# Kernel optimization log

Hardware: AMD Instinct MI355X
Metric: run time of the kernel (lower is better)

## Reference

```python
import jax, jax.numpy as jnp
import numpy as np
from jax import lax

K = 7          # neighborhood kernel size
NUM_HEADS = 4
EPS = 1e-5


def layernorm(x, w, b):
    mu = x.mean(-1, keepdims=True)
    var = ((x - mu) ** 2).mean(-1, keepdims=True)
    return (x - mu) * lax.rsqrt(var + EPS) * w + b


def window_idx(n, k):
    # NATTEN border behavior: window is shifted (not shrunk) at edges.
    start = jnp.clip(jnp.arange(n) - k // 2, 0, n - k)
    return start[:, None] + jnp.arange(k)  # [n, k]


def neighborhood_attention(x, qkv_w, qkv_b, rpb, proj_w, proj_b):
    B, H, W, C = x.shape
    nh, k = NUM_HEADS, K
    hd = C // nh
    scale = hd ** -0.5
    qkv = (x @ qkv_w + qkv_b).reshape(B, H, W, 3, nh, hd)
    q = jnp.transpose(qkv[:, :, :, 0], (0, 3, 1, 2, 4)) * scale  # [B,nh,H,W,hd]
    kk = jnp.transpose(qkv[:, :, :, 1], (0, 3, 1, 2, 4))
    vv = jnp.transpose(qkv[:, :, :, 2], (0, 3, 1, 2, 4))

    ri = window_idx(H, k)  # [H,k]
    ci = window_idx(W, k)  # [W,k]

    def gather(t):  # [B,nh,H,W,hd] -> [B,nh,H,W,k,k,hd]
        t = t[:, :, ri]           # [B,nh,H,k,W,hd]
        t = t[:, :, :, :, ci]     # [B,nh,H,k,W,k,hd]
        return jnp.transpose(t, (0, 1, 2, 4, 3, 5, 6))

    k_nb = gather(kk)
    v_nb = gather(vv).reshape(B, nh, H, W, k * k, hd)

    attn = jnp.einsum('bnhwd,bnhwijd->bnhwij', q, k_nb)  # [B,nh,H,W,k,k]

    # relative positional bias, rpb: [nh, 2k-1, 2k-1]
    br = ri - jnp.arange(H)[:, None] + (k - 1)  # [H,k] in [0, 2k-2]
    bc = ci - jnp.arange(W)[:, None] + (k - 1)  # [W,k]
    bias = rpb[:, br]                 # [nh,H,k,2k-1]
    bias = bias[:, :, :, bc]          # [nh,H,k,W,k]
    bias = jnp.transpose(bias, (0, 1, 3, 2, 4))  # [nh,H,W,k,k]

    attn = jax.nn.softmax((attn + bias[None]).reshape(B, nh, H, W, k * k), axis=-1)
    out = jnp.einsum('bnhwl,bnhwld->bnhwd', attn, v_nb)
    out = jnp.transpose(out, (0, 2, 3, 1, 4)).reshape(B, H, W, C)
    return out @ proj_w + proj_b


def mlp(x, w1, b1, w2, b2):
    return jax.nn.gelu(x @ w1 + b1, approximate=False) @ w2 + b2


def nat_block_forward(x, norm1_w, norm1_b, qkv_w, qkv_b, rpb, proj_w, proj_b,
                      norm2_w, norm2_b, fc1_w, fc1_b, fc2_w, fc2_b,
                      conv_w, dnorm_w, dnorm_b):
    depth = norm1_w.shape[0]
    for i in range(depth):
        h = layernorm(x, norm1_w[i], norm1_b[i])
        h = neighborhood_attention(h, qkv_w[i], qkv_b[i], rpb[i], proj_w[i], proj_b[i])
        x = x + h
        x = x + mlp(layernorm(x, norm2_w[i], norm2_b[i]),
                    fc1_w[i], fc1_b[i], fc2_w[i], fc2_b[i])
    # ConvDownsampler: 3x3 stride-2 conv (no bias) + LayerNorm, channels-last
    y = lax.conv_general_dilated(x, conv_w, (2, 2), ((1, 1), (1, 1)),
                                 dimension_numbers=('NHWC', 'HWIO', 'NHWC'))
    y = layernorm(y, dnorm_w, dnorm_b)
    return (y, x)


def setup_inputs() -> dict:
    key = jax.random.key(0)
    ks = jax.random.split(key, 12)
    B, H, W, C = 2, 56, 56, 128
    depth, nh, k = 2, NUM_HEADS, K
    hidden = 4 * C
    init = lambda kk, shape: jax.random.normal(kk, shape, jnp.float32) * 0.02
    return {
        'x': jax.random.normal(ks[0], (B, H, W, C), jnp.float32),
        'norm1_w': jnp.ones((depth, C), jnp.float32),
        'norm1_b': jnp.zeros((depth, C), jnp.float32),
        'qkv_w': init(ks[1], (depth, C, 3 * C)),
        'qkv_b': jnp.zeros((depth, 3 * C), jnp.float32),
        'rpb': init(ks[2], (depth, nh, 2 * k - 1, 2 * k - 1)),
        'proj_w': init(ks[3], (depth, C, C)),
        'proj_b': jnp.zeros((depth, C), jnp.float32),
        'norm2_w': jnp.ones((depth, C), jnp.float32),
        'norm2_b': jnp.zeros((depth, C), jnp.float32),
        'fc1_w': init(ks[4], (depth, C, hidden)),
        'fc1_b': jnp.zeros((depth, hidden), jnp.float32),
        'fc2_w': init(ks[5], (depth, hidden, C)),
        'fc2_b': jnp.zeros((depth, C), jnp.float32),
        'conv_w': init(ks[6], (3, 3, C, 2 * C)),
        'dnorm_w': jnp.ones((2 * C,), jnp.float32),
        'dnorm_b': jnp.zeros((2 * C,), jnp.float32),
    }


def reference(x, norm1_w, norm1_b, qkv_w, qkv_b, rpb, proj_w, proj_b,
              norm2_w, norm2_b, fc1_w, fc1_b, fc2_w, fc2_b,
              conv_w, dnorm_w, dnorm_b):
    return nat_block_forward(x, norm1_w, norm1_b, qkv_w, qkv_b, rpb, proj_w,
                             proj_b, norm2_w, norm2_b, fc1_w, fc1_b, fc2_w,
                             fc2_b, conv_w, dnorm_w, dnorm_b)
```

## Files before the change

kernel.cpp:

```cpp
#include <hip/hip_runtime.h>
#include <stdint.h>


typedef __attribute__((ext_vector_type(8))) short bf16x8;
typedef __attribute__((ext_vector_type(4))) float f32x4;

__device__ __forceinline__ float bf2f(uint16_t u) {
  union { uint32_t u; float f; } t;
  t.u = (uint32_t)u << 16;
  return t.f;
}
__device__ __forceinline__ uint16_t f2bf(float f) {
  union { float f; uint32_t u; } t;
  t.f = f;
  return (uint16_t)((t.u + 0x7FFFu + ((t.u >> 16) & 1u)) >> 16);
}

struct PrepArgs {
  const float* src[9];
  uint16_t* dst[9];
  int K[9], N[9];
  int cum[10];
};

__global__ __launch_bounds__(256) void prep_weights(PrepArgs a) {
  __shared__ float t[32][33];
  int bt = blockIdx.x;
  int j = 0;
#pragma unroll
  for (int u = 0; u < 9; ++u)
    if (bt >= a.cum[u + 1]) j = u + 1;
  int lt = bt - a.cum[j];
  const float* w = a.src[j];
  uint16_t* wt = a.dst[j];
  int K = a.K[j], N = a.N[j];
  int tn = N >> 5;
  int n0 = (lt % tn) * 32, k0 = (lt / tn) * 32;
  int tx = threadIdx.x & 31, ty = threadIdx.x >> 5;
#pragma unroll
  for (int r2 = 0; r2 < 32; r2 += 8)
    t[ty + r2][tx] = w[(size_t)(k0 + ty + r2) * N + n0 + tx];
  __syncthreads();
#pragma unroll
  for (int r2 = 0; r2 < 32; r2 += 8)
    wt[(size_t)(n0 + ty + r2) * K + k0 + tx] = f2bf(t[tx][ty + r2]);
}

__global__ __launch_bounds__(256) void ln256_kernel(const float* __restrict__ p0,
                                                    const float* __restrict__ p1,
                                                    const float* __restrict__ p2,
                                                    float* __restrict__ out,
                                                    const float* __restrict__ w,
                                                    const float* __restrict__ b) {
  int wave = threadIdx.x >> 6, lane = threadIdx.x & 63;
  int pix = blockIdx.x * 4 + wave;
  size_t base = (size_t)pix * 256;
  float v0 = p0[base + lane] + p1[base + lane] + p2[base + lane];
  float v1 = p0[base + lane + 64] + p1[base + lane + 64] + p2[base + lane + 64];
  float v2 = p0[base + lane + 128] + p1[base + lane + 128] + p2[base + lane + 128];
  float v3 = p0[base + lane + 192] + p1[base + lane + 192] + p2[base + lane + 192];
  float s = v0 + v1 + v2 + v3;
  float s2 = v0 * v0 + v1 * v1 + v2 * v2 + v3 * v3;
#pragma unroll
  for (int off = 32; off; off >>= 1) {
    s += __shfl_xor(s, off, 64);
    s2 += __shfl_xor(s2, off, 64);
  }
  float mu = s * (1.f / 256.f);
  float var = s2 * (1.f / 256.f) - mu * mu;
  float r = rsqrtf(var + 1e-5f);
  float* q = out + base;
  q[lane] = (v0 - mu) * r * w[lane] + b[lane];
  q[lane + 64] = (v1 - mu) * r * w[lane + 64] + b[lane + 64];
  q[lane + 128] = (v2 - mu) * r * w[lane + 128] + b[lane + 128];
  q[lane + 192] = (v3 - mu) * r * w[lane + 192] + b[lane + 192];
}

template <int KD, int ND, int ACT, int RES, int OUTB, int LNF>
__global__ __launch_bounds__(256) void mfma_gemm32(
    const uint16_t* __restrict__ A, const float* __restrict__ Af,
    const float* __restrict__ lnw, const float* __restrict__ lnb,
    const uint16_t* __restrict__ Wt, const float* __restrict__ bias,
    const float* __restrict__ res, float* __restrict__ outf,
    uint16_t* __restrict__ outb, float* __restrict__ outf2, int M) {
  __shared__ __align__(16) char smem[26112];
  uint16_t(*sA)[136] = (uint16_t(*)[136])smem;
  uint16_t(*sB)[136] = (uint16_t(*)[136])(smem + 8704);
  float(*sC)[68] = (float(*)[68])smem;

  int m0 = blockIdx.x * 32, n0 = blockIdx.y * 64;
  int tid = threadIdx.x, lane = tid & 63, wid = tid >> 6;
  int wr = (wid >> 1) * 16, wc = (wid & 1) * 32;
  int lc = lane & 15, g = lane >> 4;
  int lko = g * 8;

  f32x4 acc0 = {0.f, 0.f, 0.f, 0.f}, acc1 = acc0;

  constexpr int NCH = KD / 128;
#pragma unroll
  for (int c = 0; c < NCH; ++c) {
    if constexpr (LNF) {
      int r = tid >> 3, qt = tid & 7;
      const float4* xr = (const float4*)(Af + (size_t)(m0 + r) * 128 + qt * 16);
      float4 xv[4];
      float s = 0.f, s2 = 0.f;
#pragma unroll
      for (int u = 0; u < 4; ++u) {
        xv[u] = xr[u];
        s += xv[u].x + xv[u].y + xv[u].z + xv[u].w;
        s2 += xv[u].x * xv[u].x + xv[u].y * xv[u].y + xv[u].z * xv[u].z + xv[u].w * xv[u].w;
      }
      s += __shfl_xor(s, 1, 64);
      s += __shfl_xor(s, 2, 64);
      s += __shfl_xor(s, 4, 64);
      s2 += __shfl_xor(s2, 1, 64);
      s2 += __shfl_xor(s2, 2, 64);
      s2 += __shfl_xor(s2, 4, 64);
      float mu = s * (1.f / 128.f);
      float var = s2 * (1.f / 128.f) - mu * mu;
      float rstd = rsqrtf(var + 1e-5f);
      const float* lw = lnw + qt * 16;
      const float* lb = lnb + qt * 16;
      union { uint16_t us[8]; bf16x8 v; } tq[2];
#pragma unroll
      for (int u = 0; u < 4; ++u) {
        tq[u >> 1].us[(u & 1) * 4 + 0] = f2bf((xv[u].x - mu) * rstd * lw[u * 4 + 0] + lb[u * 4 + 0]);
        tq[u >> 1].us[(u & 1) * 4 + 1] = f2bf((xv[u].y - mu) * rstd * lw[u * 4 + 1] + lb[u * 4 + 1]);
        tq[u >> 1].us[(u & 1) * 4 + 2] = f2bf((xv[u].z - mu) * rstd * lw[u * 4 + 2] + lb[u * 4 + 2]);
        tq[u >> 1].us[(u & 1) * 4 + 3] = f2bf((xv[u].w - mu) * rstd * lw[u * 4 + 3] + lb[u * 4 + 3]);
      }
      *(bf16x8*)&sA[r][qt * 16] = tq[0].v;
      *(bf16x8*)&sA[r][qt * 16 + 8] = tq[1].v;
    } else {
#pragma unroll
      for (int it = 0; it < 2; ++it) {
        int chunk = tid + it * 256;
        int row = chunk >> 4, kc = (chunk & 15) * 8;
        *(bf16x8*)&sA[row][kc] =
            *(const bf16x8*)(A + (size_t)(m0 + row) * KD + c * 128 + kc);
      }
    }
#pragma unroll
    for (int it = 0; it < 4; ++it) {
      int chunk = tid + it * 256;
      int row = chunk >> 4, kc = (chunk & 15) * 8;
      *(bf16x8*)&sB[row][kc] =
          *(const bf16x8*)(Wt + (size_t)(n0 + row) * KD + c * 128 + kc);
    }
    __syncthreads();
#pragma unroll
    for (int kk = 0; kk < 128; kk += 32) {
      bf16x8 a0 = *(const bf16x8*)&sA[wr + lc][kk + lko];
      bf16x8 b0 = *(const bf16x8*)&sB[wc + lc][kk + lko];
      bf16x8 b1 = *(const bf16x8*)&sB[wc + 16 + lc][kk + lko];
      acc0 = __builtin_amdgcn_mfma_f32_16x16x32_bf16(a0, b0, acc0, 0, 0, 0);
      acc1 = __builtin_amdgcn_mfma_f32_16x16x32_bf16(a0, b1, acc1, 0, 0, 0);
    }
    __syncthreads();
  }

  {
    float bv0 = bias ? bias[n0 + wc + lc] : 0.f;
    float bv1 = bias ? bias[n0 + wc + lc + 16] : 0.f;
#pragma unroll
    for (int ni = 0; ni < 2; ++ni) {
      float bv = ni ? bv1 : bv0;
      f32x4 av = ni ? acc1 : acc0;
#pragma unroll
      for (int j = 0; j < 4; ++j) {
        float a = av[j] + bv;
        if (ACT) a = 0.5f * a * (1.f + erff(a * 0.70710678118654752f));
        sC[wr + g * 4 + j][wc + ni * 16 + lc] = a;
      }
    }
    __syncthreads();
    int r = tid >> 3, cs = (tid & 7) * 8;
    int grow = m0 + r;
    if (grow < M) {
      const float4* cp = (const float4*)&sC[r][cs];
      float4 c4[2] = {cp[0], cp[1]};
      if (RES) {
        const float4* rp = (const float4*)(res + (size_t)grow * ND + n0 + cs);
#pragma unroll
        for (int u = 0; u < 2; ++u) {
          float4 rv = rp[u];
          c4[u].x += rv.x; c4[u].y += rv.y; c4[u].z += rv.z; c4[u].w += rv.w;
        }
      }
      if (OUTB) {
        union { uint16_t us[8]; bf16x8 v; } t;
#pragma unroll
        for (int u = 0; u < 2; ++u) {
          t.us[u * 4 + 0] = f2bf(c4[u].x);
          t.us[u * 4 + 1] = f2bf(c4[u].y);
          t.us[u * 4 + 2] = f2bf(c4[u].z);
          t.us[u * 4 + 3] = f2bf(c4[u].w);
        }
        *(bf16x8*)(outb + (size_t)grow * ND + n0 + cs) = t.v;
      } else {
        float4* op = (float4*)(outf + (size_t)grow * ND + n0 + cs);
        op[0] = c4[0];
        op[1] = c4[1];
        if (outf2) {
          float4* op2 = (float4*)(outf2 + (size_t)grow * ND + n0 + cs);
          op2[0] = c4[0];
          op2[1] = c4[1];
        }
      }
    }
  }
}

#define KSWZ(row, colbytes) (((row) * 64 + (colbytes)) ^ (((row) & 7) << 4))

__global__ __launch_bounds__(256) void natten_mfma(const uint16_t* __restrict__ qkv,
                                                   const float* __restrict__ rpb,
                                                   uint16_t* __restrict__ out) {
  __shared__ uint16_t s_k[224 * 32];
  __shared__ uint16_t s_vt[32][232];
  __shared__ uint16_t s_p[64][232];
  __shared__ float s_rpb[169];

  int tid = threadIdx.x;
  int blk = blockIdx.x;
  int bh = blk & 7, tile = blk >> 3;
  int b = bh >> 2, head = bh & 3;
  int ti = tile / 7, tj = tile % 7;
  int i0 = ti * 8, j0 = tj * 8;
  int rbase = min(max(i0 - 3, 0), 42);
  int cbase = min(max(j0 - 3, 0), 42);

  const bf16x8 bz = {0, 0, 0, 0, 0, 0, 0, 0};
  const f32x4 fz = {0.f, 0.f, 0.f, 0.f};

  if (tid < 112)
    *(bf16x8*)((char*)s_k + KSWZ(196 + (tid >> 2), (tid & 3) * 16)) = bz;
  for (int idx = tid; idx < 1024; idx += 256) s_vt[idx >> 5][196 + (idx & 31)] = 0;
  for (int idx = tid; idx < 784; idx += 256) {
    int pos = idx >> 2, ch = (idx & 3) * 8;
    int r = rbase + pos / 14, c = cbase + pos % 14;
    const uint16_t* base = qkv + ((size_t)(b * 3136 + r * 56 + c)) * 384 + head * 32 + ch;
    bf16x8 kv = *(const bf16x8*)(base + 128);
    bf16x8 vv = *(const bf16x8*)(base + 256);
    *(bf16x8*)((char*)s_k + KSWZ(pos, ch * 2)) = kv;
#pragma unroll
    for (int e = 0; e < 8; ++e) s_vt[ch + e][pos] = (uint16_t)vv[e];
  }
  for (int idx = tid; idx < 169; idx += 256) s_rpb[idx] = rpb[head * 169 + idx];
  __syncthreads();

  int lane = tid & 63, wq = tid >> 6;
  int lc = lane & 15, g = lane >> 4;
  int q0 = wq * 16;

  int pA = q0 + lc;
  int piA = i0 + (pA >> 3), pjA = j0 + (pA & 7);
  bf16x8 qfrag =
      *(const bf16x8*)(qkv + ((size_t)(b * 3136 + piA * 56 + pjA)) * 384 + head * 32 + g * 8);

  f32x4 S[14];
#pragma unroll
  for (int t = 0; t < 14; ++t) {
    bf16x8 kfrag = *(const bf16x8*)((char*)s_k + KSWZ(t * 16 + lc, g * 16));
    S[t] = __builtin_amdgcn_mfma_f32_16x16x32_bf16(qfrag, kfrag, fz, 0, 0, 0);
  }

  int qi = wq * 2 + (g >> 1);
  int i = i0 + qi;
  int a = min(max(i - 3, 0), 49) - rbase;
  int brc = 6 - (i0 - rbase) - qi;
  int bj[4], bcc[4];
#pragma unroll
  for (int jj = 0; jj < 4; ++jj) {
    int qj = 4 * (g & 1) + jj;
    int j = j0 + qj;
    bj[jj] = min(max(j - 3, 0), 49) - cbase;
    bcc[jj] = 6 - (j0 - cbase) - qj;
  }

  float mx[4] = {-1e30f, -1e30f, -1e30f, -1e30f};
  int kr = (lc >= 14) ? 1 : 0;
  int kc = lc - 14 * kr;
#pragma unroll
  for (int t = 0; t < 14; ++t) {
    bool vr = (kr >= a) && (kr <= a + 6);
    int brrow = (kr + brc) * 13;
#pragma unroll
    for (int jj = 0; jj < 4; ++jj) {
      float sv = S[t][jj] * 0.17677669529663687f;
      bool v = vr && (kc >= bj[jj]) && (kc <= bj[jj] + 6);
      int bidx = v ? (brrow + kc + bcc[jj]) : 0;
      float val = v ? (sv + s_rpb[bidx]) : -1e30f;
      S[t][jj] = val;
      mx[jj] = fmaxf(mx[jj], val);
    }
    kr += 1;
    kc += 2;
    if (kc >= 14) { kc -= 14; kr += 1; }
  }
#pragma unroll
  for (int jj = 0; jj < 4; ++jj) {
#pragma unroll
    for (int off = 1; off < 16; off <<= 1) mx[jj] = fmaxf(mx[jj], __shfl_xor(mx[jj], off, 64));
  }

  float sm[4] = {0.f, 0.f, 0.f, 0.f};
#pragma unroll
  for (int t = 0; t < 14; ++t) {
#pragma unroll
    for (int jj = 0; jj < 4; ++jj) {
      float e = __expf(S[t][jj] - mx[jj]);
      sm[jj] += e;
      s_p[q0 + g * 4 + jj][t * 16 + lc] = f2bf(e);
    }
  }
#pragma unroll
  for (int jj = 0; jj < 4; ++jj) {
#pragma unroll
    for (int off = 1; off < 16; off <<= 1) sm[jj] += __shfl_xor(sm[jj], off, 64);
    sm[jj] = 1.f / sm[jj];
  }

  __syncthreads();

  f32x4 O[2] = {fz, fz};
#pragma unroll
  for (int k7 = 0; k7 < 7; ++k7) {
    bf16x8 pa = *(const bf16x8*)&s_p[q0 + lc][k7 * 32 + g * 8];
#pragma unroll
    for (int dt = 0; dt < 2; ++dt) {
      bf16x8 vb = *(const bf16x8*)&s_vt[dt * 16 + lc][k7 * 32 + g * 8];
      O[dt] = __builtin_amdgcn_mfma_f32_16x16x32_bf16(pa, vb, O[dt], 0, 0, 0);
    }
  }

#pragma unroll
  for (int jj = 0; jj < 4; ++jj) {
    int q = q0 + g * 4 + jj;
    int pi = i0 + (q >> 3), pj = j0 + (q & 7);
    size_t ob = ((size_t)(b * 3136 + pi * 56 + pj)) * 128 + head * 32;
    out[ob + lc] = f2bf(O[0][jj] * sm[jj]);
    out[ob + 16 + lc] = f2bf(O[1][jj] * sm[jj]);
  }
}

__global__ __launch_bounds__(256) void conv_gemm32(const float* __restrict__ x,
                                                   const uint16_t* __restrict__ Wt,
                                                   float* __restrict__ parts) {
  __shared__ __align__(16) char smem[26112];
  uint16_t(*sA)[136] = (uint16_t(*)[136])smem;
  uint16_t(*sB)[136] = (uint16_t(*)[136])(smem + 8704);
  float(*sC)[68] = (float(*)[68])smem;

  int m0 = blockIdx.x * 32, n0 = blockIdx.y * 64, kh = blockIdx.z;
  float* part = parts + (size_t)kh * 1568 * 256;
  int tid = threadIdx.x, lane = tid & 63, wid = tid >> 6;
  int wr = (wid >> 1) * 16, wc = (wid & 1) * 32;
  int lc = lane & 15, g = lane >> 4;
  int lko = g * 8;

  f32x4 acc0 = {0.f, 0.f, 0.f, 0.f}, acc1 = acc0;

  int r = tid >> 3, qt = tid & 7;
  int opix = m0 + r;
  int ow = opix % 28, oh = (opix / 28) % 28, bb = opix / 784;
  int ih = 2 * oh - 1 + kh;
  bool rowok = (ih >= 0) && (ih < 56);

#pragma unroll
  for (int kwc = 0; kwc < 3; ++kwc) {
    int iw = 2 * ow - 1 + kwc;
    float4 xv[4] = {{0.f, 0.f, 0.f, 0.f}, {0.f, 0.f, 0.f, 0.f},
                    {0.f, 0.f, 0.f, 0.f}, {0.f, 0.f, 0.f, 0.f}};
    if (rowok && iw >= 0 && iw < 56) {
      const float4* p =
          (const float4*)(x + (size_t)((bb * 56 + ih) * 56 + iw) * 128 + qt * 16);
#pragma unroll
      for (int u = 0; u < 4; ++u) xv[u] = p[u];
    }
    union { uint16_t us[8]; bf16x8 v; } tq[2];
#pragma unroll
    for (int u = 0; u < 4; ++u) {
      tq[u >> 1].us[(u & 1) * 4 + 0] = f2bf(xv[u].x);
      tq[u >> 1].us[(u & 1) * 4 + 1] = f2bf(xv[u].y);
      tq[u >> 1].us[(u & 1) * 4 + 2] = f2bf(xv[u].z);
      tq[u >> 1].us[(u & 1) * 4 + 3] = f2bf(xv[u].w);
    }
    *(bf16x8*)&sA[r][qt * 16] = tq[0].v;
    *(bf16x8*)&sA[r][qt * 16 + 8] = tq[1].v;
#pragma unroll
    for (int it = 0; it < 4; ++it) {
      int chunk = tid + it * 256;
      int row = chunk >> 4, kc = (chunk & 15) * 8;
      *(bf16x8*)&sB[row][kc] =
          *(const bf16x8*)(Wt + (size_t)(n0 + row) * 1152 + kh * 384 + kwc * 128 + kc);
    }
    __syncthreads();
#pragma unroll
    for (int kk = 0; kk < 128; kk += 32) {
      bf16x8 a0 = *(const bf16x8*)&sA[wr + lc][kk + lko];
      bf16x8 b0 = *(const bf16x8*)&sB[wc + lc][kk + lko];
      bf16x8 b1 = *(const bf16x8*)&sB[wc + 16 + lc][kk + lko];
      acc0 = __builtin_amdgcn_mfma_f32_16x16x32_bf16(a0, b0, acc0, 0, 0, 0);
      acc1 = __builtin_amdgcn_mfma_f32_16x16x32_bf16(a0, b1, acc1, 0, 0, 0);
    }
    __syncthreads();
  }

#pragma unroll
  for (int ni = 0; ni < 2; ++ni) {
    f32x4 av = ni ? acc1 : acc0;
#pragma unroll
    for (int j = 0; j < 4; ++j) sC[wr + g * 4 + j][wc + ni * 16 + lc] = av[j];
  }
  __syncthreads();
  int rr = tid >> 3, cs = (tid & 7) * 8;
  int grow = m0 + rr;
  if (grow < 1568) {
    const float4* cp = (const float4*)&sC[rr][cs];
    float4* op = (float4*)(part + (size_t)grow * 256 + n0 + cs);
    op[0] = cp[0];
    op[1] = cp[1];
  }
}

extern "C" void kernel_launch(void* const* d_in, const int* in_sizes, int n_in,
                              void* d_out, int out_size, void* d_ws, size_t ws_size,
                              hipStream_t stream) {
  const float* x    = (const float*)d_in[0];
  const float* n1w  = (const float*)d_in[1];
  const float* n1b  = (const float*)d_in[2];
  const float* qkvw = (const float*)d_in[3];
  const float* qkvb = (const float*)d_in[4];
  const float* rpb  = (const float*)d_in[5];
  const float* pw   = (const float*)d_in[6];
  const float* pb   = (const float*)d_in[7];
  const float* n2w  = (const float*)d_in[8];
  const float* n2b  = (const float*)d_in[9];
  const float* f1w  = (const float*)d_in[10];
  const float* f1b  = (const float*)d_in[11];
  const float* f2w  = (const float*)d_in[12];
  const float* f2b  = (const float*)d_in[13];
  const float* cw   = (const float*)d_in[14];
  const float* dnw  = (const float*)d_in[15];
  const float* dnb  = (const float*)d_in[16];
  float* out = (float*)d_out;

  char* wsb = (char*)d_ws;
  float*    xbuf    = (float*)(wsb + 0);
  uint16_t* qkv_b   = (uint16_t*)(wsb + 3211264);
  uint16_t* att_b   = (uint16_t*)(wsb + 8028160);
  uint16_t* hid_b   = (uint16_t*)(wsb + 9633792);
  float*    parts   = (float*)(wsb + 16056320);
  uint16_t* wts     = (uint16_t*)(wsb + 20873216);
  uint16_t* qkvwt = wts;
  uint16_t* pwt   = wts + 98304;
  uint16_t* f1wt  = wts + 131072;
  uint16_t* f2wt  = wts + 262144;
  uint16_t* cwt   = wts + 393216;

  PrepArgs pa;
  pa.src[0] = qkvw;         pa.dst[0] = qkvwt;          pa.K[0] = 128; pa.N[0] = 384;
  pa.src[1] = qkvw + 49152; pa.dst[1] = qkvwt + 49152;  pa.K[1] = 128; pa.N[1] = 384;
  pa.src[2] = pw;           pa.dst[2] = pwt;            pa.K[2] = 128; pa.N[2] = 128;
  pa.src[3] = pw + 16384;   pa.dst[3] = pwt + 16384;    pa.K[3] = 128; pa.N[3] = 128;
  pa.src[4] = f1w;          pa.dst[4] = f1wt;           pa.K[4] = 128; pa.N[4] = 512;
  pa.src[5] = f1w + 65536;  pa.dst[5] = f1wt + 65536;   pa.K[5] = 128; pa.N[5] = 512;
  pa.src[6] = f2w;          pa.dst[6] = f2wt;           pa.K[6] = 512; pa.N[6] = 128;
  pa.src[7] = f2w + 65536;  pa.dst[7] = f2wt + 65536;   pa.K[7] = 512; pa.N[7] = 128;
  pa.src[8] = cw;           pa.dst[8] = cwt;            pa.K[8] = 1152; pa.N[8] = 256;
  int cums[10] = {0, 48, 96, 112, 128, 192, 256, 320, 384, 672};
  for (int u = 0; u < 10; ++u) pa.cum[u] = cums[u];
  prep_weights<<<672, 256, 0, stream>>>(pa);

  for (int i = 0; i < 2; ++i) {
    const float* xin = (i == 0) ? x : xbuf;
    mfma_gemm32<128, 384, 0, 0, 1, 1><<<dim3(196, 6), 256, 0, stream>>>(
        nullptr, xin, n1w + i * 128, n1b + i * 128, qkvwt + i * 49152, qkvb + i * 384,
        nullptr, nullptr, qkv_b, nullptr, 6272);
    natten_mfma<<<392, 256, 0, stream>>>(qkv_b, rpb + i * 676, att_b);
    mfma_gemm32<128, 128, 0, 1, 0, 0><<<dim3(196, 2), 256, 0, stream>>>(
        att_b, nullptr, nullptr, nullptr, pwt + i * 16384, pb + i * 128,
        xin, xbuf, nullptr, nullptr, 6272);
    mfma_gemm32<128, 512, 1, 0, 1, 1><<<dim3(196, 8), 256, 0, stream>>>(
        nullptr, xbuf, n2w + i * 128, n2b + i * 128, f1wt + i * 65536, f1b + i * 512,
        nullptr, nullptr, hid_b, nullptr, 6272);
    mfma_gemm32<512, 128, 0, 1, 0, 0><<<dim3(196, 2), 256, 0, stream>>>(
        hid_b, nullptr, nullptr, nullptr, f2wt + i * 65536, f2b + i * 128,
        xbuf, xbuf, nullptr, (i == 1) ? (out + 401408) : nullptr, 6272);
  }

  conv_gemm32<<<dim3(49, 4, 3), 256, 0, stream>>>(xbuf, cwt, parts);
  ln256_kernel<<<392, 256, 0, stream>>>(parts, parts + 401408, parts + 802816, out, dnw, dnb);
}
```

Before: 101.6 us.

## Fuse projection, residual, LayerNorm, MLP and residual into one kernel

```diff
diff --git a/kernel.cpp b/kernel.cpp
--- a/kernel.cpp
+++ b/kernel.cpp
@@ -206,6 +206,164 @@
           op2[0] = c4[0];
           op2[1] = c4[1];
         }
+      }
+    }
+  }
+}
+
+__global__ __launch_bounds__(256) void mlp_fused(
+    const uint16_t* __restrict__ att,
+    const float* __restrict__ xin,
+    const uint16_t* __restrict__ pwt,
+    const float* __restrict__ pb,
+    const float* __restrict__ n2w, const float* __restrict__ n2b,
+    const uint16_t* __restrict__ f1wt,
+    const float* __restrict__ f1b,
+    const uint16_t* __restrict__ f2wt,
+    const float* __restrict__ f2b,
+    float* __restrict__ xout,
+    float* __restrict__ out2) {
+  __shared__ __align__(16) uint16_t sA[32][136];
+  __shared__ __align__(16) float sY[32][132];
+  __shared__ __align__(16) char sHraw[33280];
+  uint16_t(*sH)[520] = (uint16_t(*)[520])sHraw;
+  float(*sC)[132] = (float(*)[132])sHraw;
+
+  int m0 = blockIdx.x * 32;
+  int tid = threadIdx.x, lane = tid & 63, wid = tid >> 6;
+  int lc = lane & 15, g = lane >> 4;
+  int wr = (wid >> 1) * 16, wc = (wid & 1) * 64;
+  int rr = tid >> 3, qq = tid & 7;
+
+  const f32x4 fz = {0.f, 0.f, 0.f, 0.f};
+
+  const float4* rp = (const float4*)(xin + (size_t)(m0 + rr) * 128 + qq * 16);
+  float4 rv0 = rp[0], rv1 = rp[1], rv2 = rp[2], rv3 = rp[3];
+
+  {
+    const bf16x8* src = (const bf16x8*)(att + (size_t)(m0 + rr) * 128 + qq * 16);
+    *(bf16x8*)&sA[rr][qq * 16] = src[0];
+    *(bf16x8*)&sA[rr][qq * 16 + 8] = src[1];
+  }
+  __syncthreads();
+
+  f32x4 accP[4] = {fz, fz, fz, fz};
+#pragma unroll
+  for (int ks = 0; ks < 4; ++ks) {
+    bf16x8 a = *(const bf16x8*)&sA[wr + lc][ks * 32 + g * 8];
+#pragma unroll
+    for (int nt = 0; nt < 4; ++nt) {
+      int n = wc + nt * 16 + lc;
+      bf16x8 b = *(const bf16x8*)(pwt + (size_t)n * 128 + ks * 32 + g * 8);
+      accP[nt] = __builtin_amdgcn_mfma_f32_16x16x32_bf16(a, b, accP[nt], 0, 0, 0);
+    }
+  }
+#pragma unroll
+  for (int nt = 0; nt < 4; ++nt) {
+    float bv = pb[wc + nt * 16 + lc];
+#pragma unroll
+    for (int j = 0; j < 4; ++j)
+      sY[wr + g * 4 + j][wc + nt * 16 + lc] = accP[nt][j] + bv;
+  }
+  __syncthreads();
+
+  {
+    float4 v[4];
+    const float4 rvs[4] = {rv0, rv1, rv2, rv3};
+    float s = 0.f, s2 = 0.f;
+#pragma unroll
+    for (int u = 0; u < 4; ++u) {
+      float4 sv = *(const float4*)&sY[rr][qq * 16 + u * 4];
+      v[u].x = sv.x + rvs[u].x; v[u].y = sv.y + rvs[u].y;
+      v[u].z = sv.z + rvs[u].z; v[u].w = sv.w + rvs[u].w;
+      s += v[u].x + v[u].y + v[u].z + v[u].w;
+      s2 += v[u].x * v[u].x + v[u].y * v[u].y + v[u].z * v[u].z + v[u].w * v[u].w;
+    }
+    s += __shfl_xor(s, 1, 64);
+    s += __shfl_xor(s, 2, 64);
+    s += __shfl_xor(s, 4, 64);
+    s2 += __shfl_xor(s2, 1, 64);
+    s2 += __shfl_xor(s2, 2, 64);
+    s2 += __shfl_xor(s2, 4, 64);
+    float mu = s * (1.f / 128.f);
+    float var = s2 * (1.f / 128.f) - mu * mu;
+    float rstd = rsqrtf(var + 1e-5f);
+#pragma unroll
+    for (int u = 0; u < 4; ++u) *(float4*)&sY[rr][qq * 16 + u * 4] = v[u];
+    const float* lw = n2w + qq * 16;
+    const float* lb = n2b + qq * 16;
+    union { uint16_t us[8]; bf16x8 v8; } tq[2];
+#pragma unroll
+    for (int u = 0; u < 4; ++u) {
+      float* pv = (float*)&v[u];
+#pragma unroll
+      for (int e = 0; e < 4; ++e)
+        tq[u >> 1].us[(u & 1) * 4 + e] = f2bf((pv[e] - mu) * rstd * lw[u * 4 + e] + lb[u * 4 + e]);
+    }
+    *(bf16x8*)&sA[rr][qq * 16] = tq[0].v8;
+    *(bf16x8*)&sA[rr][qq * 16 + 8] = tq[1].v8;
+  }
+  __syncthreads();
+
+  int wc2 = (wid & 1) * 256;
+  f32x4 accH[16];
+#pragma unroll
+  for (int nt = 0; nt < 16; ++nt) accH[nt] = fz;
+#pragma unroll
+  for (int ks = 0; ks < 4; ++ks) {
+    bf16x8 a = *(const bf16x8*)&sA[wr + lc][ks * 32 + g * 8];
+#pragma unroll
+    for (int nt = 0; nt < 16; ++nt) {
+      int n = wc2 + nt * 16 + lc;
+      bf16x8 b = *(const bf16x8*)(f1wt + (size_t)n * 128 + ks * 32 + g * 8);
+      accH[nt] = __builtin_amdgcn_mfma_f32_16x16x32_bf16(a, b, accH[nt], 0, 0, 0);
+    }
+  }
+#pragma unroll
+  for (int nt = 0; nt < 16; ++nt) {
+    float bv = f1b[wc2 + nt * 16 + lc];
+#pragma unroll
+    for (int j = 0; j < 4; ++j) {
+      float h = accH[nt][j] + bv;
+      h = 0.5f * h * (1.f + erff(h * 0.70710678118654752f));
+      sH[wr + g * 4 + j][wc2 + nt * 16 + lc] = f2bf(h);
+    }
+  }
+  __syncthreads();
+
+  f32x4 accO[4] = {fz, fz, fz, fz};
+#pragma unroll
+  for (int ks = 0; ks < 16; ++ks) {
+    bf16x8 a = *(const bf16x8*)&sH[wr + lc][ks * 32 + g * 8];
+#pragma unroll
+    for (int nt = 0; nt < 4; ++nt) {
+      int n = wc + nt * 16 + lc;
+      bf16x8 b = *(const bf16x8*)(f2wt + (size_t)n * 512 + ks * 32 + g * 8);
+      accO[nt] = __builtin_amdgcn_mfma_f32_16x16x32_bf16(a, b, accO[nt], 0, 0, 0);
+    }
+  }
+  __syncthreads();
+#pragma unroll
+  for (int nt = 0; nt < 4; ++nt) {
+    float bv = f2b[wc + nt * 16 + lc];
+#pragma unroll
+    for (int j = 0; j < 4; ++j)
+      sC[wr + g * 4 + j][wc + nt * 16 + lc] = accO[nt][j] + bv;
+  }
+  __syncthreads();
+
+  {
+    float4* op = (float4*)(xout + (size_t)(m0 + rr) * 128 + qq * 16);
+#pragma unroll
+    for (int u = 0; u < 4; ++u) {
+      float4 cv = *(const float4*)&sC[rr][qq * 16 + u * 4];
+      float4 yv = *(const float4*)&sY[rr][qq * 16 + u * 4];
+      float4 o;
+      o.x = cv.x + yv.x; o.y = cv.y + yv.y; o.z = cv.z + yv.z; o.w = cv.w + yv.w;
+      op[u] = o;
+      if (out2) {
+        float4* op2 = (float4*)(out2 + (size_t)(m0 + rr) * 128 + qq * 16);
+        op2[u] = o;
       }
     }
   }
@@ -450,7 +608,6 @@
   float*    xbuf    = (float*)(wsb + 0);
   uint16_t* qkv_b   = (uint16_t*)(wsb + 3211264);
   uint16_t* att_b   = (uint16_t*)(wsb + 8028160);
-  uint16_t* hid_b   = (uint16_t*)(wsb + 9633792);
   float*    parts   = (float*)(wsb + 16056320);
   uint16_t* wts     = (uint16_t*)(wsb + 20873216);
   uint16_t* qkvwt = wts;
@@ -479,15 +636,10 @@
         nullptr, xin, n1w + i * 128, n1b + i * 128, qkvwt + i * 49152, qkvb + i * 384,
         nullptr, nullptr, qkv_b, nullptr, 6272);
     natten_mfma<<<392, 256, 0, stream>>>(qkv_b, rpb + i * 676, att_b);
-    mfma_gemm32<128, 128, 0, 1, 0, 0><<<dim3(196, 2), 256, 0, stream>>>(
-        att_b, nullptr, nullptr, nullptr, pwt + i * 16384, pb + i * 128,
-        xin, xbuf, nullptr, nullptr, 6272);
-    mfma_gemm32<128, 512, 1, 0, 1, 1><<<dim3(196, 8), 256, 0, stream>>>(
-        nullptr, xbuf, n2w + i * 128, n2b + i * 128, f1wt + i * 65536, f1b + i * 512,
-        nullptr, nullptr, hid_b, nullptr, 6272);
-    mfma_gemm32<512, 128, 0, 1, 0, 0><<<dim3(196, 2), 256, 0, stream>>>(
-        hid_b, nullptr, nullptr, nullptr, f2wt + i * 65536, f2b + i * 128,
-        xbuf, xbuf, nullptr, (i == 1) ? (out + 401408) : nullptr, 6272);
+    mlp_fused<<<196, 256, 0, stream>>>(
+        att_b, xin, pwt + i * 16384, pb + i * 128, n2w + i * 128, n2b + i * 128,
+        f1wt + i * 65536, f1b + i * 512, f2wt + i * 65536, f2b + i * 128,
+        xbuf, (i == 1) ? (out + 401408) : nullptr);
   }
 
   conv_gemm32<<<dim3(49, 4, 3), 256, 0, stream>>>(xbuf, cwt, parts);
```

Result: slower. 115.4 us (+13.6%).
